# Performance work log

Hardware: AMD Instinct MI355X
Metric: run time of the kernel (lower is better)

## Reference

```python
import jax, jax.numpy as jnp
import numpy as np

D_HIDDEN = 1024
N_HEAD = 16
D_HEAD = D_HIDDEN // N_HEAD  # 64
B, F = 4, 2048


def setup_inputs() -> dict:
    key = jax.random.key(0)
    ks = jax.random.split(key, 10)
    std = 0.02
    inp = {
        "q": jax.random.normal(ks[0], (B, F, D_HIDDEN), jnp.float32),
        "k": jax.random.normal(ks[1], (B, F, D_HIDDEN), jnp.float32),
        "v": jax.random.normal(ks[2], (B, F, D_HIDDEN), jnp.float32),
        # additive mask: 1 = masked position (scaled by -1e9 inside); all-zero = no masking
        "attention_mask": jnp.zeros((B, F, F), jnp.float32),
        # Dense layer params (Keras Dense: y = x @ W + b)
        "qw_w": jax.random.truncated_normal(ks[3], -2, 2, (D_HIDDEN, D_HIDDEN), jnp.float32) * std,
        "qw_b": jnp.zeros((D_HIDDEN,), jnp.float32),
        "kw_w": jax.random.truncated_normal(ks[4], -2, 2, (D_HIDDEN, D_HIDDEN), jnp.float32) * std,
        "kw_b": jnp.zeros((D_HIDDEN,), jnp.float32),
        "vw_w": jax.random.truncated_normal(ks[5], -2, 2, (D_HIDDEN, D_HIDDEN), jnp.float32) * std,
        "vw_b": jnp.zeros((D_HIDDEN,), jnp.float32),
        # output projection kernel (n_head, d_head, d_hidden)
        "out_kernel": jax.random.truncated_normal(ks[6], -2, 2, (N_HEAD, D_HEAD, D_HIDDEN), jnp.float32) * std,
    }
    return inp


def reference(q, k, v, attention_mask, qw_w, qw_b, kw_w, kw_b, vw_w, vw_b, out_kernel):
    b, f, _ = q.shape
    # linear projections
    qh = q @ qw_w + qw_b
    kh = k @ kw_w + kw_b
    vh = v @ vw_w + vw_b
    # split heads: [B, F, H, D] -> [B, H, F, D]
    def split(x):
        return x.reshape(b, -1, N_HEAD, D_HEAD).transpose(0, 2, 1, 3)
    qh, kh, vh = split(qh), split(kh), split(vh)
    # scaled dot-product attention with additive mask (1 -> -1e9)
    scores = jnp.einsum('BNFD,BNfD->BNFf', qh, kh) / jnp.sqrt(jnp.asarray(D_HEAD, qh.dtype))
    scores = scores + attention_mask[:, None, :, :] * jnp.asarray(-1e9, scores.dtype)
    probs = jax.nn.softmax(scores, axis=-1)
    out = jnp.einsum('BNFf,BNfD->BNFD', probs, vh)
    out = out.transpose(0, 2, 1, 3)  # BNFD -> BFND
    return jnp.einsum('BFND,NDM->BFM', out, out_kernel)
```

## Files before the change

kernel.cpp:

```cpp
#include <hip/hip_runtime.h>


typedef unsigned short u16;
typedef __attribute__((ext_vector_type(8))) short short8;
typedef __attribute__((ext_vector_type(4))) float f32x4;
typedef __attribute__((ext_vector_type(16))) float f32x16;

#define SC2 0.18033688011112042f
#define MSC -1.4426950408889634e9f
#define THR 8.0f

__device__ __forceinline__ u16 f2bf(float x) {
  unsigned int u = __float_as_uint(x);
  u += 0x7FFFu + ((u >> 16) & 1u);
  return (u16)(u >> 16);
}

__device__ __forceinline__ void gload16(const void* g, void* l) {
  __builtin_amdgcn_global_load_lds(
      (const __attribute__((address_space(1))) void*)g,
      (__attribute__((address_space(3))) void*)l, 16, 0, 0);
}

__device__ __forceinline__ uint4 pack8(const u16* t) {
  uint4 o;
  o.x = (unsigned)t[0] | ((unsigned)t[1] << 16);
  o.y = (unsigned)t[2] | ((unsigned)t[3] << 16);
  o.z = (unsigned)t[4] | ((unsigned)t[5] << 16);
  o.w = (unsigned)t[6] | ((unsigned)t[7] << 16);
  return o;
}

__device__ __forceinline__ unsigned cvtpk(float lo, float hi) {
  unsigned r;
  asm("v_cvt_pk_bf16_f32 %0, %1, %2" : "=v"(r) : "v"(lo), "v"(hi));
  return r;
}

__global__ __launch_bounds__(256) void cvt3(const float* __restrict__ q,
                                            const float* __restrict__ k,
                                            const float* __restrict__ v,
                                            u16* __restrict__ dq,
                                            u16* __restrict__ dk,
                                            u16* __restrict__ dv) {
  const float* s;
  u16* d;
  switch (blockIdx.y) {
    case 0: s = q; d = dq; break;
    case 1: s = k; d = dk; break;
    default: s = v; d = dv; break;
  }
  int i = blockIdx.x * 256 + threadIdx.x;
  const float4* sp = (const float4*)s;
  float4 a = sp[2 * i], b = sp[2 * i + 1];
  uint4 o;
  o.x = (unsigned)f2bf(a.x) | ((unsigned)f2bf(a.y) << 16);
  o.y = (unsigned)f2bf(a.z) | ((unsigned)f2bf(a.w) << 16);
  o.z = (unsigned)f2bf(b.x) | ((unsigned)f2bf(b.y) << 16);
  o.w = (unsigned)f2bf(b.z) | ((unsigned)f2bf(b.w) << 16);
  ((uint4*)d)[i] = o;
}

__global__ __launch_bounds__(256) void masksum(const float* __restrict__ mask,
                                               unsigned char* __restrict__ msum) {
  int t = blockIdx.x * 256 + threadIdx.x;
  int row = t & 2047;
  int kt = (t >> 11) & 31;
  int b = t >> 16;
  const float4* p =
      (const float4*)(mask + ((size_t)(b * 2048 + row)) * 2048 + kt * 64);
  unsigned acc = 0;
#pragma unroll
  for (int i = 0; i < 16; i++) {
    float4 f = p[i];
    acc |= __float_as_uint(f.x) | __float_as_uint(f.y) |
           __float_as_uint(f.z) | __float_as_uint(f.w);
  }
  msum[t] = acc ? 1 : 0;
}

__global__ __launch_bounds__(256) void wtrans(
    const float* __restrict__ w0, const float* __restrict__ w1,
    const float* __restrict__ w2, const float* __restrict__ w3,
    u16* __restrict__ o0, u16* __restrict__ o1,
    u16* __restrict__ o2, u16* __restrict__ o3) {
  const float* W; u16* O;
  switch (blockIdx.z) {
    case 0: W = w0; O = o0; break;
    case 1: W = w1; O = o1; break;
    case 2: W = w2; O = o2; break;
    default: W = w3; O = o3; break;
  }
  __shared__ u16 T[64][72];
  const int t = threadIdx.x, r = t >> 2, seg = t & 3;
  const int k0 = blockIdx.y * 64, n0 = blockIdx.x * 64;
  const float* src = W + (size_t)(k0 + r) * 1024 + n0 + seg * 16;
#pragma unroll
  for (int jj = 0; jj < 4; jj++) {
    float4 f = ((const float4*)src)[jj];
    T[r][seg * 16 + jj * 4 + 0] = f2bf(f.x);
    T[r][seg * 16 + jj * 4 + 1] = f2bf(f.y);
    T[r][seg * 16 + jj * 4 + 2] = f2bf(f.z);
    T[r][seg * 16 + jj * 4 + 3] = f2bf(f.w);
  }
  __syncthreads();
  u16 tmp[16];
#pragma unroll
  for (int j = 0; j < 16; j++) tmp[j] = T[seg * 16 + j][r];
  u16* dst = O + (size_t)(n0 + r) * 1024 + k0 + seg * 16;
  ((uint4*)dst)[0] = pack8(tmp);
  ((uint4*)dst)[1] = pack8(tmp + 8);
}

__global__ __launch_bounds__(256) void vtrans(const u16* __restrict__ vh,
                                              u16* __restrict__ vhT) {
  const int bh = blockIdx.y, f0 = blockIdx.x * 64;
  const int b = bh >> 4, h = bh & 15;
  __shared__ u16 T[64][72];
  const int t = threadIdx.x, r = t >> 2, seg = t & 3;
  const u16* src = vh + (size_t)(b * 2048 + f0 + r) * 1024 + h * 64 + seg * 16;
  uint4 v0 = ((const uint4*)src)[0], v1 = ((const uint4*)src)[1];
  *(uint4*)&T[r][seg * 16] = v0;
  *(uint4*)&T[r][seg * 16 + 8] = v1;
  __syncthreads();
  u16 tmp[16];
#pragma unroll
  for (int j = 0; j < 16; j++) tmp[j] = T[seg * 16 + j][r];
  u16* dst = vhT + (size_t)(bh * 64 + r) * 2048 + f0 + seg * 16;
  ((uint4*)dst)[0] = pack8(tmp);
  ((uint4*)dst)[1] = pack8(tmp + 8);
}

__global__ __launch_bounds__(256) void gemm128(
    const u16* __restrict__ A, const u16* __restrict__ Bt,
    const float* __restrict__ bias, void* __restrict__ Cout, int cfp32,
    float scl) {
  constexpr int K = 1024, N = 1024;
  __shared__ u16 lsA[128 * 32];
  __shared__ u16 lsB[128 * 32];
  const int tid = threadIdx.x;
  const int w = tid >> 6, lane = tid & 63;
  const int l15 = lane & 15, lg = lane >> 4;
  const int m0 = blockIdx.y << 7, n0 = blockIdx.x << 7;
  const int wr = w >> 1, wc = w & 1;

  f32x4 acc[4][4];
#pragma unroll
  for (int i = 0; i < 4; i++)
#pragma unroll
    for (int j = 0; j < 4; j++) acc[i][j] = f32x4{0.f, 0.f, 0.f, 0.f};

  const u16* As = A + (size_t)(m0 + w * 32 + (lane >> 2)) * K + (lane & 3) * 8;
  const u16* Bs = Bt + (size_t)(n0 + w * 32 + (lane >> 2)) * K + (lane & 3) * 8;
  u16* lA = &lsA[(w * 32) * 32];
  u16* lB = &lsB[(w * 32) * 32];

  for (int k0 = 0; k0 < K; k0 += 32) {
    gload16(As + k0, lA);
    gload16(As + 16 * K + k0, lA + 16 * 32);
    gload16(Bs + k0, lB);
    gload16(Bs + 16 * K + k0, lB + 16 * 32);
    __syncthreads();
    short8 af[4], bfv[4];
#pragma unroll
    for (int mi = 0; mi < 4; mi++)
      af[mi] = *(const short8*)&lsA[(wr * 64 + mi * 16 + l15) * 32 + lg * 8];
#pragma unroll
    for (int nj = 0; nj < 4; nj++)
      bfv[nj] = *(const short8*)&lsB[(wc * 64 + nj * 16 + l15) * 32 + lg * 8];
#pragma unroll
    for (int mi = 0; mi < 4; mi++)
#pragma unroll
      for (int nj = 0; nj < 4; nj++)
        acc[mi][nj] = __builtin_amdgcn_mfma_f32_16x16x32_bf16(af[mi], bfv[nj],
                                                              acc[mi][nj], 0, 0, 0);
    __syncthreads();
  }

  const int crow = m0 + wr * 64 + lg * 4;
  const int ccol = n0 + wc * 64 + l15;
  if (cfp32) {
    float* C = (float*)Cout;
#pragma unroll
    for (int nj = 0; nj < 4; nj++)
#pragma unroll
      for (int mi = 0; mi < 4; mi++)
#pragma unroll
        for (int r = 0; r < 4; r++)
          C[(size_t)(crow + mi * 16 + r) * N + ccol + nj * 16] = acc[mi][nj][r];
  } else {
    u16* C = (u16*)Cout;
#pragma unroll
    for (int nj = 0; nj < 4; nj++) {
      float bv = bias[ccol + nj * 16];
#pragma unroll
      for (int mi = 0; mi < 4; mi++)
#pragma unroll
        for (int r = 0; r < 4; r++)
          C[(size_t)(crow + mi * 16 + r) * N + ccol + nj * 16] =
              f2bf((acc[mi][nj][r] + bv) * scl);
    }
  }
}

__global__ __launch_bounds__(256, 4) void attn_fwd(
    const u16* __restrict__ qh, const u16* __restrict__ kh,
    const u16* __restrict__ vhT, const float* __restrict__ mask,
    const unsigned char* __restrict__ msum, u16* __restrict__ aout) {
  __shared__ u16 Kls[2][64][72];
  __shared__ u16 Vls[2][64][72];

  const int tid = threadIdx.x;
  const int w = tid >> 6, lane = tid & 63;
  const int l31 = lane & 31, hi = lane >> 5;
  const int blk = ((blockIdx.x & 7) << 7) | (blockIdx.x >> 3);
  const int qt = blk & 15, bh = blk >> 4, h = bh & 15, b = bh >> 4;
  const int frow = qt * 128 + w * 32;
  const size_t qrow0 = (size_t)b * 2048 + frow;

  short8 qf[4];
#pragma unroll
  for (int ds = 0; ds < 4; ds++)
    qf[ds] = *(const short8*)&qh[(qrow0 + l31) * 1024 + h * 64 + ds * 16 + hi * 8];

  f32x16 oacc[2];
#pragma unroll
  for (int i = 0; i < 16; i++) { oacc[0][i] = 0.f; oacc[1][i] = 0.f; }
  float m_run = 0.f, l_run = 0.f;

  const int sr = tid >> 2, seg = tid & 3;
  const u16* Ksrc = kh + ((size_t)b * 2048 + sr) * 1024 + h * 64 + seg * 16;
  const u16* Vsrc = vhT + ((size_t)bh * 64 + sr) * 2048 + seg * 16;
  const unsigned char* msrow = msum + (size_t)b * 65536 + frow + l31;

  uint4 ka0, ka1, va0, va1;
  unsigned char mb, mbn;
  {
    const uint4* kp = (const uint4*)Ksrc;
    uint4 x0 = kp[0], x1 = kp[1];
    const uint4* vp = (const uint4*)Vsrc;
    uint4 y0 = vp[0], y1 = vp[1];
    *(uint4*)&Kls[0][sr][seg * 16] = x0;
    *(uint4*)&Kls[0][sr][seg * 16 + 8] = x1;
    *(uint4*)&Vls[0][sr][seg * 16] = y0;
    *(uint4*)&Vls[0][sr][seg * 16 + 8] = y1;
    kp = (const uint4*)(Ksrc + 64 * 1024);
    ka0 = kp[0]; ka1 = kp[1];
    vp = (const uint4*)(Vsrc + 64);
    va0 = vp[0]; va1 = vp[1];
    mb = msrow[0];
    mbn = msrow[2048];
  }
  __syncthreads();

  for (int kt = 0; kt < 32; kt++) {
    const int cur = kt & 1;
    const int k0 = kt * 64;
    const int mflag = __any((int)mb);
    mb = mbn;

    if (kt < 31) {
      *(uint4*)&Kls[cur ^ 1][sr][seg * 16] = ka0;
      *(uint4*)&Kls[cur ^ 1][sr][seg * 16 + 8] = ka1;
      *(uint4*)&Vls[cur ^ 1][sr][seg * 16] = va0;
      *(uint4*)&Vls[cur ^ 1][sr][seg * 16 + 8] = va1;
    }
    if (kt < 30) {
      const uint4* kp = (const uint4*)(Ksrc + (size_t)(kt + 2) * 64 * 1024);
      ka0 = kp[0]; ka1 = kp[1];
      const uint4* vp = (const uint4*)(Vsrc + (kt + 2) * 64);
      va0 = vp[0]; va1 = vp[1];
      mbn = msrow[(size_t)(kt + 2) * 2048];
    }

    f32x16 sacc[2];
#pragma unroll
    for (int i = 0; i < 16; i++) { sacc[0][i] = 0.f; sacc[1][i] = 0.f; }
#pragma unroll
    for (int kb = 0; kb < 2; kb++) {
      short8 kf[4];
#pragma unroll
      for (int ds = 0; ds < 4; ds++)
        kf[ds] = *(const short8*)&Kls[cur][kb * 32 + l31][ds * 16 + hi * 8];
      __builtin_amdgcn_s_setprio(1);
#pragma unroll
      for (int ds = 0; ds < 4; ds++)
        sacc[kb] = __builtin_amdgcn_mfma_f32_32x32x16_bf16(kf[ds], qf[ds],
                                                           sacc[kb], 0, 0, 0);
      __builtin_amdgcn_s_setprio(0);
    }

    if (mflag) {
      const size_t mrow = ((size_t)b * 2048 + frow + l31) * 2048 + (size_t)k0;
#pragma unroll
      for (int kb = 0; kb < 2; kb++)
#pragma unroll
        for (int r = 0; r < 16; r++) {
          float mv = mask[mrow + kb * 32 + (r & 3) + 8 * (r >> 2) + 4 * hi];
          sacc[kb][r] = fmaf(mv, MSC, sacc[kb][r]);
        }
      float mx[16];
#pragma unroll
      for (int r = 0; r < 16; r++) mx[r] = fmaxf(sacc[0][r], sacc[1][r]);
#pragma unroll
      for (int s = 8; s >= 1; s >>= 1)
#pragma unroll
        for (int r = 0; r < s; r++) mx[r] = fmaxf(mx[r], mx[r + s]);
      float tm = mx[0];
      tm = fmaxf(tm, __shfl_xor(tm, 32, 64));
      if (!__all(tm <= m_run + THR)) {
        float mnew = fmaxf(m_run, tm);
        float al = exp2f(m_run - mnew);
        m_run = mnew;
        l_run *= al;
#pragma unroll
        for (int r = 0; r < 16; r++) {
          float alr = __shfl(al, (r & 3) + 8 * (r >> 2) + 4 * hi, 64);
          oacc[0][r] *= alr;
          oacc[1][r] *= alr;
        }
      }
    }

    float rsp = 0.f, rsq = 0.f;
    unsigned pw[16];
    if (m_run == 0.f) {
#pragma unroll
      for (int kb = 0; kb < 2; kb++)
#pragma unroll
        for (int jp = 0; jp < 2; jp++) {
          float e[8];
#pragma unroll
          for (int t = 0; t < 8; t++)
            e[t] = exp2f(sacc[kb][8 * jp + t]);
          rsp += (e[0] + e[1]) + (e[2] + e[3]);
          rsq += (e[4] + e[5]) + (e[6] + e[7]);
          unsigned ye0 = cvtpk(e[0], e[1]);
          unsigned ye1 = cvtpk(e[2], e[3]);
          unsigned xo0 = cvtpk(e[4], e[5]);
          unsigned xo1 = cvtpk(e[6], e[7]);
          asm volatile("v_permlane32_swap_b32 %0, %1" : "+v"(ye0), "+v"(xo0));
          asm volatile("v_permlane32_swap_b32 %0, %1" : "+v"(ye1), "+v"(xo1));
          const int kk = kb * 2 + jp;
          pw[kk * 4 + 0] = ye0;
          pw[kk * 4 + 1] = ye1;
          pw[kk * 4 + 2] = xo0;
          pw[kk * 4 + 3] = xo1;
        }
    } else {
      const float mm = m_run;
#pragma unroll
      for (int kb = 0; kb < 2; kb++)
#pragma unroll
        for (int jp = 0; jp < 2; jp++) {
          float e[8];
#pragma unroll
          for (int t = 0; t < 8; t++)
            e[t] = exp2f(sacc[kb][8 * jp + t] - mm);
          rsp += (e[0] + e[1]) + (e[2] + e[3]);
          rsq += (e[4] + e[5]) + (e[6] + e[7]);
          unsigned ye0 = cvtpk(e[0], e[1]);
          unsigned ye1 = cvtpk(e[2], e[3]);
          unsigned xo0 = cvtpk(e[4], e[5]);
          unsigned xo1 = cvtpk(e[6], e[7]);
          asm volatile("v_permlane32_swap_b32 %0, %1" : "+v"(ye0), "+v"(xo0));
          asm volatile("v_permlane32_swap_b32 %0, %1" : "+v"(ye1), "+v"(xo1));
          const int kk = kb * 2 + jp;
          pw[kk * 4 + 0] = ye0;
          pw[kk * 4 + 1] = ye1;
          pw[kk * 4 + 2] = xo0;
          pw[kk * 4 + 3] = xo1;
        }
    }
    float rs = rsp + rsq;
    rs += __shfl_xor(rs, 32, 64);
    l_run += rs;

#pragma unroll
    for (int dn = 0; dn < 2; dn++) {
      short8 vf[4];
#pragma unroll
      for (int kk = 0; kk < 4; kk++)
        vf[kk] = *(const short8*)&Vls[cur][dn * 32 + l31][kk * 16 + hi * 8];
      __builtin_amdgcn_s_setprio(1);
#pragma unroll
      for (int kk = 0; kk < 4; kk++) {
        uint4 t4 = {pw[kk * 4 + 0], pw[kk * 4 + 1], pw[kk * 4 + 2], pw[kk * 4 + 3]};
        oacc[dn] = __builtin_amdgcn_mfma_f32_32x32x16_bf16(
            *(short8*)&t4, vf[kk], oacc[dn], 0, 0, 0);
      }
      __builtin_amdgcn_s_setprio(0);
    }

    __syncthreads();
  }

  float inv = 1.0f / l_run;
#pragma unroll
  for (int r = 0; r < 16; r++) {
    const int qr = (r & 3) + 8 * (r >> 2) + 4 * hi;
    float invr = __shfl(inv, qr, 64);
    aout[(qrow0 + qr) * 1024 + h * 64 + l31] = f2bf(oacc[0][r] * invr);
    aout[(qrow0 + qr) * 1024 + h * 64 + 32 + l31] = f2bf(oacc[1][r] * invr);
  }
}

extern "C" void kernel_launch(void* const* d_in, const int* in_sizes, int n_in,
                              void* d_out, int out_size, void* d_ws, size_t ws_size,
                              hipStream_t stream) {
  (void)in_sizes; (void)n_in; (void)out_size; (void)ws_size;
  const float* q    = (const float*)d_in[0];
  const float* k    = (const float*)d_in[1];
  const float* v    = (const float*)d_in[2];
  const float* mask = (const float*)d_in[3];
  const float* qw_w = (const float*)d_in[4];
  const float* qw_b = (const float*)d_in[5];
  const float* kw_w = (const float*)d_in[6];
  const float* kw_b = (const float*)d_in[7];
  const float* vw_w = (const float*)d_in[8];
  const float* vw_b = (const float*)d_in[9];
  const float* wo   = (const float*)d_in[10];

  u16* qbf = (u16*)d_ws;
  u16* kbf = qbf + 8192 * 1024;
  u16* vbf = kbf + 8192 * 1024;
  u16* vh  = vbf + 8192 * 1024;
  u16* qwT = vh + 8192 * 1024;
  u16* kwT = qwT + 1024 * 1024;
  u16* vwT = kwT + 1024 * 1024;
  u16* woT = vwT + 1024 * 1024;
  u16* vhT    = qbf;
  u16* attn_o = kbf;
  unsigned char* msumb = (unsigned char*)(woT + 1024 * 1024);
  u16* qh = (u16*)d_out;
  u16* kh = qh + 8192 * 1024;

  cvt3<<<dim3(4096, 3), 256, 0, stream>>>(q, k, v, qbf, kbf, vbf);
  wtrans<<<dim3(16, 16, 4), 256, 0, stream>>>(qw_w, kw_w, vw_w, wo,
                                              qwT, kwT, vwT, woT);
  gemm128<<<dim3(8, 64), 256, 0, stream>>>(qbf, qwT, qw_b, qh, 0, SC2);
  gemm128<<<dim3(8, 64), 256, 0, stream>>>(kbf, kwT, kw_b, kh, 0, 1.0f);
  gemm128<<<dim3(8, 64), 256, 0, stream>>>(vbf, vwT, vw_b, vh, 0, 1.0f);
  vtrans<<<dim3(32, 64), 256, 0, stream>>>(vh, vhT);
  masksum<<<1024, 256, 0, stream>>>(mask, msumb);
  attn_fwd<<<1024, 256, 0, stream>>>(qh, kh, vhT, mask, msumb, attn_o);
  gemm128<<<dim3(8, 64), 256, 0, stream>>>(attn_o, woT, nullptr, d_out, 1, 1.0f);
}
```

Before: 298.5 us.

## Batch Q/K/V projections into one launch and fuse V transpose into epilogue

Merges the three separate Q, K and V projection GEMM launches into a single grid with a z dimension selecting the operand set. The V projection's epilogue now stages its tile in shared memory and writes it already transposed, so the separate vtrans kernel and the vh round trip through memory go away. The intent is to cut launch overhead, improve GPU fill with one larger grid, and remove a full read/write pass of the V activations. The cost is a larger shared buffer in the projection kernel, which may lower occupancy, and an extra LDS transpose step in the V epilogue.

```diff
diff --git a/kernel.cpp b/kernel.cpp
--- a/kernel.cpp
+++ b/kernel.cpp
@@ -112,29 +112,108 @@
   ((uint4*)dst)[1] = pack8(tmp + 8);
 }
 
-__global__ __launch_bounds__(256) void vtrans(const u16* __restrict__ vh,
-                                              u16* __restrict__ vhT) {
-  const int bh = blockIdx.y, f0 = blockIdx.x * 64;
-  const int b = bh >> 4, h = bh & 15;
-  __shared__ u16 T[64][72];
-  const int t = threadIdx.x, r = t >> 2, seg = t & 3;
-  const u16* src = vh + (size_t)(b * 2048 + f0 + r) * 1024 + h * 64 + seg * 16;
-  uint4 v0 = ((const uint4*)src)[0], v1 = ((const uint4*)src)[1];
-  *(uint4*)&T[r][seg * 16] = v0;
-  *(uint4*)&T[r][seg * 16 + 8] = v1;
-  __syncthreads();
-  u16 tmp[16];
-#pragma unroll
-  for (int j = 0; j < 16; j++) tmp[j] = T[seg * 16 + j][r];
-  u16* dst = vhT + (size_t)(bh * 64 + r) * 2048 + f0 + seg * 16;
-  ((uint4*)dst)[0] = pack8(tmp);
-  ((uint4*)dst)[1] = pack8(tmp + 8);
-}
-
-__global__ __launch_bounds__(256) void gemm128(
+__global__ __launch_bounds__(256) void gemm_proj3(
+    const u16* __restrict__ Aq, const u16* __restrict__ Ak,
+    const u16* __restrict__ Av, const u16* __restrict__ Wq,
+    const u16* __restrict__ Wk, const u16* __restrict__ Wv,
+    const float* __restrict__ bq, const float* __restrict__ bk,
+    const float* __restrict__ bv, u16* __restrict__ oq,
+    u16* __restrict__ ok, u16* __restrict__ ovT) {
+  constexpr int K = 1024, N = 1024;
+  __shared__ u16 sbuf[128 * 136];
+  u16* lsA = sbuf;
+  u16* lsB = sbuf + 128 * 32;
+  const int z = blockIdx.z;
+  const u16* A  = (z == 0) ? Aq : (z == 1) ? Ak : Av;
+  const u16* Bt = (z == 0) ? Wq : (z == 1) ? Wk : Wv;
+  const float* bias = (z == 0) ? bq : (z == 1) ? bk : bv;
+
+  const int tid = threadIdx.x;
+  const int w = tid >> 6, lane = tid & 63;
+  const int l15 = lane & 15, lg = lane >> 4;
+  const int m0 = blockIdx.y << 7, n0 = blockIdx.x << 7;
+  const int wr = w >> 1, wc = w & 1;
+
+  f32x4 acc[4][4];
+#pragma unroll
+  for (int i = 0; i < 4; i++)
+#pragma unroll
+    for (int j = 0; j < 4; j++) acc[i][j] = f32x4{0.f, 0.f, 0.f, 0.f};
+
+  const u16* As = A + (size_t)(m0 + w * 32 + (lane >> 2)) * K + (lane & 3) * 8;
+  const u16* Bs = Bt + (size_t)(n0 + w * 32 + (lane >> 2)) * K + (lane & 3) * 8;
+  u16* lA = &lsA[(w * 32) * 32];
+  u16* lB = &lsB[(w * 32) * 32];
+
+  for (int k0 = 0; k0 < K; k0 += 32) {
+    gload16(As + k0, lA);
+    gload16(As + 16 * K + k0, lA + 16 * 32);
+    gload16(Bs + k0, lB);
+    gload16(Bs + 16 * K + k0, lB + 16 * 32);
+    __syncthreads();
+    short8 af[4], bfv[4];
+#pragma unroll
+    for (int mi = 0; mi < 4; mi++)
+      af[mi] = *(const short8*)&lsA[(wr * 64 + mi * 16 + l15) * 32 + lg * 8];
+#pragma unroll
+    for (int nj = 0; nj < 4; nj++)
+      bfv[nj] = *(const short8*)&lsB[(wc * 64 + nj * 16 + l15) * 32 + lg * 8];
+#pragma unroll
+    for (int mi = 0; mi < 4; mi++)
+#pragma unroll
+      for (int nj = 0; nj < 4; nj++)
+        acc[mi][nj] = __builtin_amdgcn_mfma_f32_16x16x32_bf16(af[mi], bfv[nj],
+                                                              acc[mi][nj], 0, 0, 0);
+    __syncthreads();
+  }
+
+  const int crow = m0 + wr * 64 + lg * 4;
+  const int ccol = n0 + wc * 64 + l15;
+  if (z < 2) {
+    u16* C = (z == 0) ? oq : ok;
+    const float scl = (z == 0) ? SC2 : 1.0f;
+#pragma unroll
+    for (int nj = 0; nj < 4; nj++) {
+      float bv = bias[ccol + nj * 16];
+#pragma unroll
+      for (int mi = 0; mi < 4; mi++)
+#pragma unroll
+        for (int r = 0; r < 4; r++)
+          C[(size_t)(crow + mi * 16 + r) * N + ccol + nj * 16] =
+              f2bf((acc[mi][nj][r] + bv) * scl);
+    }
+  } else {
+    const int rl = wr * 64 + lg * 4;
+    const int cl = wc * 64 + l15;
+#pragma unroll
+    for (int nj = 0; nj < 4; nj++) {
+      float bv = bias[ccol + nj * 16];
+#pragma unroll
+      for (int mi = 0; mi < 4; mi++)
+#pragma unroll
+        for (int r = 0; r < 4; r++)
+          sbuf[(rl + mi * 16 + r) * 136 + cl + nj * 16] =
+              f2bf(acc[mi][nj][r] + bv);
+    }
+    __syncthreads();
+    const int drow = tid >> 1, seg = tid & 1;
+    const int b = m0 >> 11;
+    const int f0 = (m0 & 2047) + seg * 64;
+    u16* dst = ovT + (size_t)(b * 1024 + n0 + drow) * 2048 + f0;
+#pragma unroll
+    for (int c = 0; c < 8; c++) {
+      u16 tmp[8];
+#pragma unroll
+      for (int j = 0; j < 8; j++)
+        tmp[j] = sbuf[(seg * 64 + c * 8 + j) * 136 + drow];
+      ((uint4*)dst)[c] = pack8(tmp);
+    }
+  }
+}
+
+__global__ __launch_bounds__(256) void gemm_out(
     const u16* __restrict__ A, const u16* __restrict__ Bt,
-    const float* __restrict__ bias, void* __restrict__ Cout, int cfp32,
-    float scl) {
+    float* __restrict__ C) {
   constexpr int K = 1024, N = 1024;
   __shared__ u16 lsA[128 * 32];
   __shared__ u16 lsB[128 * 32];
@@ -179,28 +258,13 @@
 
   const int crow = m0 + wr * 64 + lg * 4;
   const int ccol = n0 + wc * 64 + l15;
-  if (cfp32) {
-    float* C = (float*)Cout;
-#pragma unroll
-    for (int nj = 0; nj < 4; nj++)
-#pragma unroll
-      for (int mi = 0; mi < 4; mi++)
-#pragma unroll
-        for (int r = 0; r < 4; r++)
-          C[(size_t)(crow + mi * 16 + r) * N + ccol + nj * 16] = acc[mi][nj][r];
-  } else {
-    u16* C = (u16*)Cout;
-#pragma unroll
-    for (int nj = 0; nj < 4; nj++) {
-      float bv = bias[ccol + nj * 16];
-#pragma unroll
-      for (int mi = 0; mi < 4; mi++)
-#pragma unroll
-        for (int r = 0; r < 4; r++)
-          C[(size_t)(crow + mi * 16 + r) * N + ccol + nj * 16] =
-              f2bf((acc[mi][nj][r] + bv) * scl);
-    }
-  }
+#pragma unroll
+  for (int nj = 0; nj < 4; nj++)
+#pragma unroll
+    for (int mi = 0; mi < 4; mi++)
+#pragma unroll
+      for (int r = 0; r < 4; r++)
+        C[(size_t)(crow + mi * 16 + r) * N + ccol + nj * 16] = acc[mi][nj][r];
 }
 
 __global__ __launch_bounds__(256, 4) void attn_fwd(
@@ -424,12 +488,11 @@
   u16* qbf = (u16*)d_ws;
   u16* kbf = qbf + 8192 * 1024;
   u16* vbf = kbf + 8192 * 1024;
-  u16* vh  = vbf + 8192 * 1024;
-  u16* qwT = vh + 8192 * 1024;
+  u16* vhT = vbf + 8192 * 1024;
+  u16* qwT = vhT + 8192 * 1024;
   u16* kwT = qwT + 1024 * 1024;
   u16* vwT = kwT + 1024 * 1024;
   u16* woT = vwT + 1024 * 1024;
-  u16* vhT    = qbf;
   u16* attn_o = kbf;
   unsigned char* msumb = (unsigned char*)(woT + 1024 * 1024);
   u16* qh = (u16*)d_out;
@@ -438,11 +501,9 @@
   cvt3<<<dim3(4096, 3), 256, 0, stream>>>(q, k, v, qbf, kbf, vbf);
   wtrans<<<dim3(16, 16, 4), 256, 0, stream>>>(qw_w, kw_w, vw_w, wo,
                                               qwT, kwT, vwT, woT);
-  gemm128<<<dim3(8, 64), 256, 0, stream>>>(qbf, qwT, qw_b, qh, 0, SC2);
-  gemm128<<<dim3(8, 64), 256, 0, stream>>>(kbf, kwT, kw_b, kh, 0, 1.0f);
-  gemm128<<<dim3(8, 64), 256, 0, stream>>>(vbf, vwT, vw_b, vh, 0, 1.0f);
-  vtrans<<<dim3(32, 64), 256, 0, stream>>>(vh, vhT);
+  gemm_proj3<<<dim3(8, 64, 3), 256, 0, stream>>>(qbf, kbf, vbf, qwT, kwT, vwT,
+                                                 qw_b, kw_b, vw_b, qh, kh, vhT);
   masksum<<<1024, 256, 0, stream>>>(mask, msumb);
   attn_fwd<<<1024, 256, 0, stream>>>(qh, kh, vhT, mask, msumb, attn_o);
-  gemm128<<<dim3(8, 64), 256, 0, stream>>>(attn_o, woT, nullptr, d_out, 1, 1.0f);
-}
+  gemm_out<<<dim3(8, 64), 256, 0, stream>>>(attn_o, woT, (float*)d_out);
+}
```

Result: faster. 276.4 us (median of 2 runs) (-7.4%).
